# Kernel optimization log

Hardware: AMD Instinct MI355X
Metric: run time of the kernel (lower is better)

## Reference

```python
import jax, jax.numpy as jnp
import numpy as np

C = 128
B = 64
EPS = 1e-6


def _ln2d(x, w, b):
    # LayerNorm over channel dim (NAFNet-style LayerNorm2d), eps=1e-6
    mu = x.mean(axis=1, keepdims=True)
    var = ((x - mu) ** 2).mean(axis=1, keepdims=True)
    return (x - mu) / jnp.sqrt(var + EPS) * w[None, :, None, None] + b[None, :, None, None]


def _conv4(x, w, b):
    # Conv2d kernel 4, stride 4, no padding; NCHW / OIHW
    y = jax.lax.conv_general_dilated(x, w, (4, 4), 'VALID',
                                     dimension_numbers=('NCHW', 'OIHW', 'NCHW'))
    return y + b[None, :, None, None]


def _pixel_shuffle4(x):
    # (B, c*16, H, W) -> (B, c, 4H, 4W), torch PixelShuffle semantics
    b, c16, h, w = x.shape
    c = c16 // 16
    x = x.reshape(b, c, 4, 4, h, w)
    x = x.transpose(0, 1, 4, 2, 5, 3)
    return x.reshape(b, c, h * 4, w * 4)


def setup_inputs() -> dict:
    key = jax.random.key(0)
    ks = jax.random.split(key, 16)
    s = 0.02
    return {
        'x_l': jax.random.normal(ks[0], (B, C, 32, 32), jnp.float32),
        'x_r': jax.random.normal(ks[1], (B, C, 32, 32), jnp.float32),
        'ln_w_l': jnp.ones((C,), jnp.float32), 'ln_b_l': jnp.zeros((C,), jnp.float32),
        'ln_w_r': jnp.ones((C,), jnp.float32), 'ln_b_r': jnp.zeros((C,), jnp.float32),
        'Wl1': jax.random.normal(ks[2], (C, C, 4, 4), jnp.float32) * s,
        'bl1': jnp.zeros((C,), jnp.float32),
        'Wr1': jax.random.normal(ks[3], (C, C, 4, 4), jnp.float32) * s,
        'br1': jnp.zeros((C,), jnp.float32),
        'Wl2': jax.random.normal(ks[4], (C, C, 4, 4), jnp.float32) * s,
        'bl2': jnp.zeros((C,), jnp.float32),
        'Wr2': jax.random.normal(ks[5], (C, C, 4, 4), jnp.float32) * s,
        'br2': jnp.zeros((C,), jnp.float32),
        'pos': jax.random.normal(ks[6], (1, C, 8, 8), jnp.float32),
        'beta': jax.random.normal(ks[7], (1, C, 1, 1), jnp.float32) * s,
        'gamma': jax.random.normal(ks[8], (1, C, 1, 1), jnp.float32) * s,
        'Wl3': jax.random.normal(ks[9], (16 * C, C), jnp.float32) * s,
        'bl3': jnp.zeros((16 * C,), jnp.float32),
        'Wr3': jax.random.normal(ks[10], (16 * C, C), jnp.float32) * s,
        'br3': jnp.zeros((16 * C,), jnp.float32),
    }


def reference(x_l, x_r, ln_w_l, ln_b_l, ln_w_r, ln_b_r, Wl1, bl1, Wr1, br1,
              Wl2, bl2, Wr2, br2, pos, beta, gamma, Wl3, bl3, Wr3, br3):
    c = x_l.shape[1]
    scale = c ** (-0.5)
    B1 = x_l.shape[0]
    B2 = x_r.shape[0]

    Ql = _conv4(_ln2d(x_l, ln_w_l, ln_b_l), Wl1, bl1) + pos  # (B1,c,8,8)
    Qr = _conv4(_ln2d(x_r, ln_w_r, ln_b_r), Wr1, br1) + pos  # (B2,c,8,8)
    h1, w1 = Ql.shape[-2], Ql.shape[-1]
    h2, w2 = Qr.shape[-2], Qr.shape[-1]
    m1, m2 = h1 * w1, h2 * w2

    Qlm = Ql.transpose(0, 2, 3, 1).reshape(B1, m1, c)          # b (h w) c
    Qrm = Qr.transpose(1, 0, 2, 3).reshape(c, B2 * m2)         # c (b h w)
    Vl = (_conv4(x_l, Wl2, bl2) + pos).transpose(0, 2, 3, 1).reshape(B1 * m1, c)
    Vr = (_conv4(x_r, Wr2, br2) + pos).transpose(0, 2, 3, 1).reshape(B2 * m2, c)

    attn = jnp.matmul(Qlm, Qrm) * scale                        # (B1, m1, B2*m2)

    F_r2l = jnp.matmul(jax.nn.softmax(attn * (B2 ** (-0.5)), axis=-1), Vr)
    F_r2l = F_r2l.reshape(B1, h1, w1, c)

    attn2 = attn.reshape(B1, m1, B2, m2).transpose(2, 3, 0, 1).reshape(B2, m2, B1 * m1)
    F_l2r = jnp.matmul(jax.nn.softmax(attn2 * (B1 ** (-0.5)), axis=-1), Vl)
    F_l2r = F_l2r.reshape(B2, h2, w2, c)

    F_r2l = _pixel_shuffle4((jnp.matmul(F_r2l, Wl3.T) + bl3).transpose(0, 3, 1, 2)) * beta
    F_l2r = _pixel_shuffle4((jnp.matmul(F_l2r, Wr3.T) + br3).transpose(0, 3, 1, 2)) * gamma
    return (x_l + F_r2l, x_r + F_l2r)
```

## Files before the change

kernel.cpp:

```cpp
#include <hip/hip_runtime.h>
#include <stdint.h>

using bf16x8 = __attribute__((ext_vector_type(8))) short;
using f32x4  = __attribute__((ext_vector_type(4))) float;

__device__ __forceinline__ unsigned short f2bf(float f) {
  union { float f; uint32_t u; } v; v.f = f;
  uint32_t r = v.u + 0x7FFFu + ((v.u >> 16) & 1u);
  return (unsigned short)(r >> 16);
}
__device__ __forceinline__ uint32_t pk2(float a, float b) {
  return (uint32_t)f2bf(a) | ((uint32_t)f2bf(b) << 16);
}
__device__ __forceinline__ float bf2f(unsigned short s) {
  union { uint32_t u; float f; } v; v.u = ((uint32_t)s) << 16;
  return v.f;
}
__device__ __forceinline__ f32x4 mfma16(bf16x8 a, bf16x8 b, f32x4 c) {
  return __builtin_amdgcn_mfma_f32_16x16x32_bf16(a, b, c, 0, 0, 0);
}

__global__ __launch_bounds__(256) void k_lnstats(
    const float* __restrict__ xl, const float* __restrict__ xr,
    float* __restrict__ muW, float* __restrict__ rsW)
{
  const int bx = blockIdx.x;
  const int side = bx >> 7, rem = bx & 127;
  const int b = rem >> 1, half = rem & 1;
  const float* x = (side ? xr : xl) + (size_t)b * 131072 + half * 512;
  const int t = threadIdx.x;
  const int px = t * 2;
  float s0=0, s1=0, q0=0, q1=0;
#pragma unroll 4
  for (int c = 0; c < 128; ++c) {
    const float2 v = *(const float2*)(x + c*1024 + px);
    s0 += v.x; q0 += v.x*v.x;
    s1 += v.y; q1 += v.y*v.y;
  }
  const int o = (side*64 + b)*1024 + half*512 + px;
  float2 mu, rs;
  mu.x = s0*(1.0f/128.0f); mu.y = s1*(1.0f/128.0f);
  rs.x = rsqrtf(fmaxf(q0*(1.0f/128.0f) - mu.x*mu.x, 0.0f) + 1e-6f);
  rs.y = rsqrtf(fmaxf(q1*(1.0f/128.0f) - mu.y*mu.y, 0.0f) + 1e-6f);
  *(float2*)(muW + o) = mu;
  *(float2*)(rsW + o) = rs;
}

__global__ __launch_bounds__(256) void k_wprep(
    const float* __restrict__ lnwl, const float* __restrict__ lnbl,
    const float* __restrict__ lnwr, const float* __restrict__ lnbr,
    const float* __restrict__ Wl1, const float* __restrict__ bl1,
    const float* __restrict__ Wr1, const float* __restrict__ br1,
    const float* __restrict__ Wl2, const float* __restrict__ Wr2,
    unsigned short* __restrict__ Wq, unsigned short* __restrict__ Wv,
    float* __restrict__ bqW)
{
  const int bx = blockIdx.x;
  const int side = bx >> 7, co = bx & 127;
  const float* W1  = side ? Wr1 : Wl1;
  const float* W2  = side ? Wr2 : Wl2;
  const float* b1  = side ? br1 : bl1;
  const float* lnw = side ? lnwr : lnwl;
  const float* lnb = side ? lnbr : lnbl;
  const int t = threadIdx.x;
  const int ci = t >> 1;
  const float lw = lnw[ci], lb = lnb[ci];

  const size_t dsto = (size_t)(side*32 + (t>>3))*8192 + (size_t)co*64 + (t&7)*8;

  const float* src1 = W1 + (size_t)co*2048 + t*8;
  const float4 a0 = *(const float4*)(src1);
  const float4 a1 = *(const float4*)(src1 + 4);
  float part = (a0.x+a0.y+a0.z+a0.w + a1.x+a1.y+a1.z+a1.w) * lb;
  uint4 pkq;
  pkq.x = pk2(a0.x*lw, a0.y*lw); pkq.y = pk2(a0.z*lw, a0.w*lw);
  pkq.z = pk2(a1.x*lw, a1.y*lw); pkq.w = pk2(a1.z*lw, a1.w*lw);
  *(uint4*)(Wq + dsto) = pkq;

  const float* src2 = W2 + (size_t)co*2048 + t*8;
  const float4 c0 = *(const float4*)(src2);
  const float4 c1 = *(const float4*)(src2 + 4);
  uint4 pkv;
  pkv.x = pk2(c0.x, c0.y); pkv.y = pk2(c0.z, c0.w);
  pkv.z = pk2(c1.x, c1.y); pkv.w = pk2(c1.z, c1.w);
  *(uint4*)(Wv + dsto) = pkv;

  __shared__ float red[4];
  float v = part;
  v += __shfl_down(v, 32, 64); v += __shfl_down(v, 16, 64);
  v += __shfl_down(v, 8, 64);  v += __shfl_down(v, 4, 64);
  v += __shfl_down(v, 2, 64);  v += __shfl_down(v, 1, 64);
  if ((t & 63) == 0) red[t >> 6] = v;
  __syncthreads();
  if (t == 0) bqW[side*128 + co] = b1[co] + red[0] + red[1] + red[2] + red[3];
}

__global__ __launch_bounds__(256) void k_w3prep(
    const float* __restrict__ Wl3, const float* __restrict__ Wr3,
    unsigned short* __restrict__ W3bf)
{
  const int b = blockIdx.x;
  const float* src = (b < 256 ? Wl3 : Wr3) + (size_t)(b & 255) * 1024;
  const int t = threadIdx.x;
  const float4 v = *(const float4*)(src + t*4);
  *(uint2*)(W3bf + (size_t)b*1024 + t*4) = make_uint2(pk2(v.x, v.y), pk2(v.z, v.w));
}

__global__ __launch_bounds__(256) void k_conv(
    const float* __restrict__ xl, const float* __restrict__ xr,
    const unsigned short* __restrict__ Wq, const unsigned short* __restrict__ Wv,
    const float* __restrict__ muW, const float* __restrict__ rsW,
    unsigned short* __restrict__ Cpart)
{
  const int bid = blockIdx.x;
  const int ks = bid & 3;
  const int img = (bid >> 2) & 63;
  const int ctype = bid >> 8;
  const int side = ctype & 1;
  const bool isQ = ctype < 2;
  const float* x = (side ? xr : xl) + (size_t)img * 131072;
  const unsigned short* Bsrc = (isQ ? Wq : Wv) + (size_t)side * 262144;

  const int t = threadIdx.x;
  const int w = t >> 6, l = t & 63, lo = l & 15, g = l >> 4;

  __shared__ __align__(16) unsigned char lds[24576];
  unsigned char* A = lds;
  unsigned char* B = lds + 8192;

  const int cl   = t >> 6;
  const int px0  = (t & 63) * 16;
  const int y    = px0 >> 5;
  const int wr   = y & 3;
  const int pbase = (y >> 2)*8 + ((px0 & 31) >> 2);

  float4 mu4[4], rs4[4];
  if (isQ) {
    const int o = (side*64 + img)*1024 + px0;
#pragma unroll
    for (int i = 0; i < 4; ++i) {
      mu4[i] = *(const float4*)(muW + o + 4*i);
      rs4[i] = *(const float4*)(rsW + o + 4*i);
    }
  }

  const int cout = t >> 1, part = t & 1;
  const int keyB = ((cout ^ (cout >> 3)) & 7) << 4;

  f32x4 acc[4][2];
#pragma unroll
  for (int a = 0; a < 4; ++a) { acc[a][0] = (f32x4)0.0f; acc[a][1] = (f32x4)0.0f; }

  for (int it = 0; it < 8; ++it) {
    const int kb = ks*8 + it;
    __syncthreads();
    {
      const float* xs = x + (size_t)(kb*4 + cl)*1024 + px0;
#pragma unroll
      for (int i = 0; i < 4; ++i) {
        float4 v = *(const float4*)(xs + 4*i);
        if (isQ) {
          v.x = (v.x - mu4[i].x)*rs4[i].x; v.y = (v.y - mu4[i].y)*rs4[i].y;
          v.z = (v.z - mu4[i].z)*rs4[i].z; v.w = (v.w - mu4[i].w)*rs4[i].w;
        }
        const int p = pbase + i;
        int dst = p*128 + cl*32 + wr*8;
        dst ^= ((p ^ (p >> 3)) & 7) << 4;
        *(uint2*)(A + dst) = make_uint2(pk2(v.x, v.y), pk2(v.z, v.w));
      }
    }
    {
      const unsigned short* bs = Bsrc + (size_t)kb*8192 + t*32;
#pragma unroll
      for (int i = 0; i < 4; ++i) {
        const bf16x8 v = *(const bf16x8*)(bs + i*8);
        *(bf16x8*)(B + cout*128 + ((part*64 + i*16) ^ keyB)) = v;
      }
    }
    __syncthreads();
    bf16x8 af[4][2], bfr[2][2];
#pragma unroll
    for (int mf = 0; mf < 4; ++mf) {
      const int row = mf*16 + lo;
      const int key = ((row ^ (row >> 3)) & 7) << 4;
#pragma unroll
      for (int kc = 0; kc < 2; ++kc)
        af[mf][kc] = *(const bf16x8*)(A + row*128 + ((kc*64 + g*16) ^ key));
    }
#pragma unroll
    for (int nf = 0; nf < 2; ++nf) {
      const int row = w*32 + nf*16 + lo;
      const int key = ((row ^ (row >> 3)) & 7) << 4;
#pragma unroll
      for (int kc = 0; kc < 2; ++kc)
        bfr[nf][kc] = *(const bf16x8*)(B + row*128 + ((kc*64 + g*16) ^ key));
    }
    __builtin_amdgcn_s_setprio(1);
#pragma unroll
    for (int kc = 0; kc < 2; ++kc)
#pragma unroll
      for (int nf = 0; nf < 2; ++nf)
#pragma unroll
        for (int mf = 0; mf < 4; ++mf)
          acc[mf][nf] = mfma16(af[mf][kc], bfr[nf][kc], acc[mf][nf]);
    __builtin_amdgcn_s_setprio(0);
  }

  unsigned short* Cp = Cpart + (size_t)bid * 8192;
#pragma unroll
  for (int mf = 0; mf < 4; ++mf)
#pragma unroll
    for (int nf = 0; nf < 2; ++nf) {
      const int c = w*32 + nf*16 + lo;
      const int p0 = mf*16 + g*4;
      *(uint2*)(Cp + c*64 + p0) =
          make_uint2(pk2(acc[mf][nf][0], acc[mf][nf][1]),
                     pk2(acc[mf][nf][2], acc[mf][nf][3]));
    }
}

__global__ __launch_bounds__(256) void k_convred(
    const unsigned short* __restrict__ Cpart,
    const float* __restrict__ bqW,
    const float* __restrict__ bl2, const float* __restrict__ br2,
    const float* __restrict__ pos,
    unsigned short* __restrict__ Qbf, unsigned short* __restrict__ Vtbf)
{
  const int bid2 = blockIdx.x;
  const int ctype = bid2 >> 6, img = bid2 & 63;
  const int side = ctype & 1;
  const bool isQ = ctype < 2;
  const int t = threadIdx.x;

  __shared__ float S[64][130];

  const int c = t >> 1, p0 = (t & 1) * 32;
  {
    float acc[32];
#pragma unroll
    for (int j = 0; j < 32; ++j) acc[j] = 0.f;
#pragma unroll
    for (int s = 0; s < 4; ++s) {
      const unsigned short* Cp = Cpart + ((size_t)(bid2*4 + s))*8192 + c*64 + p0;
#pragma unroll
      for (int j8 = 0; j8 < 4; ++j8) {
        const bf16x8 v = *(const bf16x8*)(Cp + j8*8);
#pragma unroll
        for (int e = 0; e < 8; ++e)
          acc[j8*8 + e] += bf2f((unsigned short)v[e]);
      }
    }
#pragma unroll
    for (int j = 0; j < 32; ++j) S[p0 + j][c] = acc[j];
  }
  __syncthreads();

  if (isQ) {
    const float* bq = bqW + side*128;
    const int p = t >> 2, c0 = (t & 3) * 32;
    const int rot = (t & 3) * 4;
    uint32_t pk[16];
#pragma unroll
    for (int j2 = 0; j2 < 16; ++j2) {
      const int jj = (j2 + rot) & 15;
      const int ca = c0 + jj*2;
      const float2 sv = *(const float2*)(&S[p][ca]);
      const float va = (sv.x + bq[ca]     + pos[ca*64 + p])     * 0.105112052f;
      const float vb = (sv.y + bq[ca + 1] + pos[(ca+1)*64 + p]) * 0.105112052f;
      pk[jj] = pk2(va, vb);
    }
    unsigned short* Qo = Qbf + (size_t)side*524288 + ((size_t)(img*64 + p))*128 + c0;
    *(uint4*)(Qo)      = make_uint4(pk[0],  pk[1],  pk[2],  pk[3]);
    *(uint4*)(Qo + 8)  = make_uint4(pk[4],  pk[5],  pk[6],  pk[7]);
    *(uint4*)(Qo + 16) = make_uint4(pk[8],  pk[9],  pk[10], pk[11]);
    *(uint4*)(Qo + 24) = make_uint4(pk[12], pk[13], pk[14], pk[15]);
  } else {
    const float* b2 = side ? br2 : bl2;
    const float bb = b2[c];
    uint32_t pk[16];
#pragma unroll
    for (int j2 = 0; j2 < 16; ++j2) {
      const int pa = p0 + j2*2;
      const float va = S[pa][c]     + bb + pos[c*64 + pa];
      const float vb = S[pa + 1][c] + bb + pos[c*64 + pa + 1];
      pk[j2] = pk2(va, vb);
    }
    unsigned short* Vo = Vtbf + (size_t)side*524288 + (size_t)c*4096 + img*64 + p0;
    *(uint4*)(Vo)      = make_uint4(pk[0],  pk[1],  pk[2],  pk[3]);
    *(uint4*)(Vo + 8)  = make_uint4(pk[4],  pk[5],  pk[6],  pk[7]);
    *(uint4*)(Vo + 16) = make_uint4(pk[8],  pk[9],  pk[10], pk[11]);
    *(uint4*)(Vo + 24) = make_uint4(pk[12], pk[13], pk[14], pk[15]);
  }
}

__global__ __launch_bounds__(256, 2) void k_attn(
    const unsigned short* __restrict__ Qbf,
    const unsigned short* __restrict__ Vtbf,
    float* __restrict__ Opart,
    float* __restrict__ Lpart)
{
  const int bid = blockIdx.x;
  const int xcd = bid & 7;
  const int dir = xcd >> 2;
  const int ks  = xcd & 3;
  const int qb  = bid >> 3;
  const unsigned short* Qp = Qbf  + (size_t)dir*524288;
  const unsigned short* Kp = Qbf  + (size_t)(1-dir)*524288;
  const unsigned short* Vp = Vtbf + (size_t)(1-dir)*524288;

  const int t = threadIdx.x;
  const int w = t >> 6, l = t & 63, lo = l & 15, g = l >> 4;

  __shared__ __align__(16) unsigned char lds[73728];
  unsigned char* ldsP = lds + 65536;
  __shared__ float lred[4][64];

  bf16x8 aq[4][4];
#pragma unroll
  for (int mf = 0; mf < 4; ++mf)
#pragma unroll
    for (int kc = 0; kc < 4; ++kc)
      aq[mf][kc] = *(const bf16x8*)(Qp + (size_t)(qb*64 + mf*16 + lo)*128 + kc*32 + g*8);

  f32x4 o[4][2];
#pragma unroll
  for (int a = 0; a < 4; ++a) { o[a][0] = (f32x4)0.0f; o[a][1] = (f32x4)0.0f; }
  float ls[4][4] = {{0,0,0,0},{0,0,0,0},{0,0,0,0},{0,0,0,0}};

  const int kt0 = ks * 16;

  const int ksrcBase = t ^ ((t >> 4) & 7);
  const int vc    = t >> 3;
  const int vi16  = (t & 7) * 16;
  const int vsoff = (vi16 ^ (((t >> 3) & 7) << 4)) >> 1;

  {
    const uint4* src = (const uint4*)(Kp + (size_t)kt0*8192);
#pragma unroll
    for (int j = 0; j < 4; ++j)
      *(uint4*)(lds + (t + 256*j)*16) = src[ksrcBase + 256*j];
#pragma unroll
    for (int j = 0; j < 4; ++j) {
      const int c = vc + 32*j;
      *(uint4*)(lds + 32768 + c*128 + vi16) =
          *(const uint4*)(Vp + (size_t)c*4096 + kt0*64 + vsoff);
    }
  }
  __syncthreads();

  for (int it = 0; it < 16; ++it) {
    const int cur = it & 1;
    unsigned char* curK = lds + cur*16384;
    unsigned char* curV = lds + 32768 + cur*16384;

    uint4 kr0, kr1, kr2, kr3, vr0, vr1, vr2, vr3;
    if (it < 15) {
      const int kt = kt0 + it + 1;
      const uint4* src = (const uint4*)(Kp + (size_t)kt*8192);
      kr0 = src[ksrcBase];
      kr1 = src[ksrcBase + 256];
      kr2 = src[ksrcBase + 512];
      kr3 = src[ksrcBase + 768];
      const unsigned short* vsrc = Vp + (size_t)kt*64 + vsoff;
      vr0 = *(const uint4*)(vsrc + (size_t)(vc     )*4096);
      vr1 = *(const uint4*)(vsrc + (size_t)(vc + 32)*4096);
      vr2 = *(const uint4*)(vsrc + (size_t)(vc + 64)*4096);
      vr3 = *(const uint4*)(vsrc + (size_t)(vc + 96)*4096);
    }

    f32x4 s[4];
    s[0] = (f32x4)0.0f; s[1] = (f32x4)0.0f; s[2] = (f32x4)0.0f; s[3] = (f32x4)0.0f;
    const int krow = w*16 + lo;
    const int keyk = (krow & 7) << 4;
    __builtin_amdgcn_s_setprio(1);
#pragma unroll
    for (int kc = 0; kc < 4; ++kc) {
      const bf16x8 bk = *(const bf16x8*)(curK + krow*256 + ((kc*64 + g*16) ^ keyk));
#pragma unroll
      for (int mf = 0; mf < 4; ++mf)
        s[mf] = mfma16(aq[mf][kc], bk, s[mf]);
    }
    __builtin_amdgcn_s_setprio(0);

#pragma unroll
    for (int mf = 0; mf < 4; ++mf)
#pragma unroll
      for (int rr = 0; rr < 4; ++rr) {
        const float e = __expf(s[mf][rr]);
        ls[mf][rr] += e;
        const int q = mf*16 + g*4 + rr;
        const int inrow = (w*32 + lo*2) ^ ((q & 7) << 4);
        *(unsigned short*)(ldsP + q*128 + inrow) = f2bf(e);
      }
    __syncthreads();

    __builtin_amdgcn_s_setprio(1);
#pragma unroll
    for (int kd = 0; kd < 2; ++kd) {
      bf16x8 pa[4];
#pragma unroll
      for (int mf = 0; mf < 4; ++mf) {
        const int q = mf*16 + lo;
        pa[mf] = *(const bf16x8*)(ldsP + q*128 + ((kd*64 + g*16) ^ ((q & 7) << 4)));
      }
#pragma unroll
      for (int nf = 0; nf < 2; ++nf) {
        const int c = w*32 + nf*16 + lo;
        const bf16x8 bv = *(const bf16x8*)(curV + c*128 + ((kd*64 + g*16) ^ ((c & 7) << 4)));
#pragma unroll
        for (int mf = 0; mf < 4; ++mf)
          o[mf][nf] = mfma16(pa[mf], bv, o[mf][nf]);
      }
    }
    __builtin_amdgcn_s_setprio(0);

    if (it < 15) {
      unsigned char* nK = lds + (cur ^ 1)*16384;
      unsigned char* nV = lds + 32768 + (cur ^ 1)*16384;
      *(uint4*)(nK + (t      )*16) = kr0;
      *(uint4*)(nK + (t + 256)*16) = kr1;
      *(uint4*)(nK + (t + 512)*16) = kr2;
      *(uint4*)(nK + (t + 768)*16) = kr3;
      *(uint4*)(nV + (vc     )*128 + vi16) = vr0;
      *(uint4*)(nV + (vc + 32)*128 + vi16) = vr1;
      *(uint4*)(nV + (vc + 64)*128 + vi16) = vr2;
      *(uint4*)(nV + (vc + 96)*128 + vi16) = vr3;
    }
    __syncthreads();
  }

#pragma unroll
  for (int mf = 0; mf < 4; ++mf)
#pragma unroll
    for (int rr = 0; rr < 4; ++rr) {
      float v = ls[mf][rr];
      v += __shfl_xor(v, 1, 64);
      v += __shfl_xor(v, 2, 64);
      v += __shfl_xor(v, 4, 64);
      v += __shfl_xor(v, 8, 64);
      ls[mf][rr] = v;
    }
  if (lo == 0) {
#pragma unroll
    for (int mf = 0; mf < 4; ++mf)
#pragma unroll
      for (int rr = 0; rr < 4; ++rr)
        lred[w][mf*16 + g*4 + rr] = ls[mf][rr];
  }
  __syncthreads();

  float* Ob = Opart + (((size_t)dir*64 + qb)*4 + ks)*64*128;
#pragma unroll
  for (int mf = 0; mf < 4; ++mf)
#pragma unroll
    for (int nf = 0; nf < 2; ++nf) {
      const int c = w*32 + nf*16 + lo;
#pragma unroll
      for (int rr = 0; rr < 4; ++rr) {
        const int q = mf*16 + g*4 + rr;
        Ob[q*128 + c] = o[mf][nf][rr];
      }
    }
  if (t < 64)
    Lpart[(((size_t)dir*64 + qb)*4 + ks)*64 + t] =
        lred[0][t] + lred[1][t] + lred[2][t] + lred[3][t];
}

__global__ __launch_bounds__(256) void k_reduce(
    const float* __restrict__ Opart, const float* __restrict__ Lpart,
    unsigned short* __restrict__ Fbf)
{
  const int bid = blockIdx.x;
  const int dir = bid >> 7, rb = bid & 127;
  const int t = threadIdx.x;
  const int qr = t >> 3;
  const int cs = (t & 7) * 16;
  const int r  = rb*32 + qr;
  const int qb = r >> 6, q = r & 63;
  const size_t pb = ((size_t)dir*64 + qb)*4;
  float acc[16];
#pragma unroll
  for (int i = 0; i < 16; ++i) acc[i] = 0.f;
  float lsum = 0.f;
#pragma unroll
  for (int s = 0; s < 4; ++s) {
    const float* Ob = Opart + ((pb + s)*64 + q)*128 + cs;
#pragma unroll
    for (int i = 0; i < 16; i += 4) {
      const float4 v = *(const float4*)(Ob + i);
      acc[i] += v.x; acc[i+1] += v.y; acc[i+2] += v.z; acc[i+3] += v.w;
    }
    lsum += Lpart[(pb + s)*64 + q];
  }
  const float inv = 1.0f / lsum;
  uint32_t pkw[8];
#pragma unroll
  for (int i = 0; i < 8; ++i) pkw[i] = pk2(acc[2*i]*inv, acc[2*i+1]*inv);
  unsigned short* Fo = Fbf + (size_t)dir*524288 + (size_t)r*128 + cs;
  *(uint4*)(Fo)     = make_uint4(pkw[0], pkw[1], pkw[2], pkw[3]);
  *(uint4*)(Fo + 8) = make_uint4(pkw[4], pkw[5], pkw[6], pkw[7]);
}

__global__ __launch_bounds__(256) void k_proj(
    const unsigned short* __restrict__ Fbf,
    const unsigned short* __restrict__ W3bf,
    const float* __restrict__ bl3, const float* __restrict__ br3,
    const float* __restrict__ beta, const float* __restrict__ gamma,
    const float* __restrict__ xl, const float* __restrict__ xr,
    float* __restrict__ out)
{
  const int nb = blockIdx.x, mb = blockIdx.y, side = blockIdx.z;
  const unsigned short* F  = Fbf + (size_t)side*524288 + (size_t)mb*8192;
  const unsigned short* W3 = W3bf + (size_t)side*262144 + (size_t)nb*16384;
  const float* b3  = (side ? br3 : bl3) + nb*128;
  const float* scl = side ? gamma : beta;
  const float* xin = (side ? xr : xl) + (size_t)mb*131072;
  float* op = out + (size_t)side*8388608 + (size_t)mb*131072;

  const int t = threadIdx.x;
  const int w = t >> 6, l = t & 63, lo = l & 15, g = l >> 4;

  __shared__ __align__(16) unsigned char lds[49152];
  unsigned char* Ft = lds;
  unsigned char* B3 = lds + 16384;
  float* Sf = (float*)lds;

  {
    const uint4* src = (const uint4*)F;
#pragma unroll
    for (int j = 0; j < 4; ++j) {
      const int idx = t + 256*j;
      const int dst = idx*16;
      const int row = dst >> 8;
      *(uint4*)(Ft + dst) = src[(dst ^ ((row & 7) << 4)) >> 4];
    }
  }
  {
    const int nl = t >> 1, half = t & 1;
    const unsigned short* wsrc = W3 + (size_t)nl*128 + half*64;
#pragma unroll
    for (int ch = 0; ch < 8; ++ch) {
      const uint4 v = *(const uint4*)(wsrc + ch*8);
      const int inrow = (half*128 + ch*16) ^ ((nl & 7) << 4);
      *(uint4*)(B3 + nl*256 + inrow) = v;
    }
  }
  __syncthreads();

  f32x4 acc[4][2];
#pragma unroll
  for (int a=0;a<4;a++) { acc[a][0] = (f32x4)0.0f; acc[a][1] = (f32x4)0.0f; }

  bf16x8 af[4][4];
#pragma unroll
  for (int mf = 0; mf < 4; ++mf) {
    const int row = mf*16 + lo;
#pragma unroll
    for (int kc = 0; kc < 4; ++kc)
      af[mf][kc] = *(const bf16x8*)(Ft + row*256 + ((kc*64 + g*16) ^ ((row & 7) << 4)));
  }
#pragma unroll
  for (int kc = 0; kc < 4; ++kc)
#pragma unroll
    for (int nf = 0; nf < 2; ++nf) {
      const int n = w*32 + nf*16 + lo;
      const bf16x8 bb = *(const bf16x8*)(B3 + n*256 + ((kc*64 + g*16) ^ ((n & 7) << 4)));
#pragma unroll
      for (int mf = 0; mf < 4; ++mf)
        acc[mf][nf] = mfma16(af[mf][kc], bb, acc[mf][nf]);
    }

  __syncthreads();

  {
    const int r4 = (lo >> 2) & 3, sc = lo & 3;
#pragma unroll
    for (int nf = 0; nf < 2; ++nf) {
      const int cl = w*2 + nf;
      const int n16 = w*32 + nf*16 + lo;
      const float scc = scl[nb*8 + cl];
      const float bb3 = b3[n16];
#pragma unroll
      for (int mf = 0; mf < 4; ++mf)
#pragma unroll
        for (int rr = 0; rr < 4; ++rr) {
          const int pi = mf*16 + g*4 + rr;
          const int h = pi >> 3, wc = pi & 7;
          Sf[cl*1032 + h*128 + r4*32 + wc*4 + sc] = scc*(acc[mf][nf][rr] + bb3);
        }
    }
  }
  __syncthreads();

#pragma unroll
  for (int j = 0; j < 8; ++j) {
    const int pix = t*4;
    const float4 s = *(const float4*)(Sf + j*1032 + pix);
    const size_t gaddr = (size_t)(nb*8 + j)*1024 + pix;
    const float4 xv = *(const float4*)(xin + gaddr);
    float4 r;
    r.x = xv.x + s.x; r.y = xv.y + s.y; r.z = xv.z + s.z; r.w = xv.w + s.w;
    *(float4*)(op + gaddr) = r;
  }
}

extern "C" void kernel_launch(void* const* d_in, const int* in_sizes, int n_in,
                              void* d_out, int out_size, void* d_ws, size_t ws_size,
                              hipStream_t stream) {
  (void)in_sizes; (void)n_in; (void)out_size; (void)ws_size;
  const float* xl   = (const float*)d_in[0];
  const float* xr   = (const float*)d_in[1];
  const float* lnwl = (const float*)d_in[2];
  const float* lnbl = (const float*)d_in[3];
  const float* lnwr = (const float*)d_in[4];
  const float* lnbr = (const float*)d_in[5];
  const float* Wl1  = (const float*)d_in[6];
  const float* bl1  = (const float*)d_in[7];
  const float* Wr1  = (const float*)d_in[8];
  const float* br1  = (const float*)d_in[9];
  const float* Wl2  = (const float*)d_in[10];
  const float* bl2  = (const float*)d_in[11];
  const float* Wr2  = (const float*)d_in[12];
  const float* br2  = (const float*)d_in[13];
  const float* pos  = (const float*)d_in[14];
  const float* beta = (const float*)d_in[15];
  const float* gamma= (const float*)d_in[16];
  const float* Wl3  = (const float*)d_in[17];
  const float* bl3  = (const float*)d_in[18];
  const float* Wr3  = (const float*)d_in[19];
  const float* br3  = (const float*)d_in[20];

  float* muW = (float*)d_ws;
  float* rsW = muW + 131072;
  float* bqW = rsW + 131072;
  unsigned short* Wq   = (unsigned short*)(bqW + 256);
  unsigned short* Wv   = Wq + 524288;
  unsigned short* Qbf  = Wv + 524288;
  unsigned short* Vtbf = Qbf + 1048576;
  unsigned short* Fbf  = Vtbf + 1048576;
  unsigned short* W3bf = Fbf + 1048576;
  unsigned short* Cpart = W3bf + 524288;
  float* Opart = (float*)Cpart;
  float* Lpart = (float*)(Cpart + 8388608);

  k_lnstats<<<256, 256, 0, stream>>>(xl, xr, muW, rsW);
  k_wprep<<<256, 256, 0, stream>>>(lnwl, lnbl, lnwr, lnbr,
      Wl1, bl1, Wr1, br1, Wl2, Wr2, Wq, Wv, bqW);
  k_w3prep<<<512, 256, 0, stream>>>(Wl3, Wr3, W3bf);
  k_conv<<<1024, 256, 0, stream>>>(xl, xr, Wq, Wv, muW, rsW, Cpart);
  k_convred<<<256, 256, 0, stream>>>(Cpart, bqW, bl2, br2, pos, Qbf, Vtbf);
  k_attn<<<512, 256, 0, stream>>>(Qbf, Vtbf, Opart, Lpart);
  k_reduce<<<256, 256, 0, stream>>>(Opart, Lpart, Fbf);
  k_proj<<<dim3(16, 64, 2), 256, 0, stream>>>(Fbf, W3bf, bl3, br3,
      beta, gamma, xl, xr, (float*)d_out);
}
```

Before: 124.9 us.

## Merge prep kernels into one launch and transpose score MFMA for packed P stores

Folds the LN-stats, conv-weight prep and projection-weight prep kernels into a single launch, removing two launch gaps. In attention the QK^T MFMA operands are swapped so each lane holds four consecutive keys of one query. The exp values can then be stored to LDS as one packed 8-byte write instead of four scalar 2-byte writes, and the row-sum reduction needs fewer shuffles. The Q scale gains a log2(e) factor so exp2f replaces __expf; this relies on matching swizzle and layout, and the merged kernel keeps a __syncthreads inside only one branch.

```diff
diff --git a/kernel.cpp b/kernel.cpp
--- a/kernel.cpp
+++ b/kernel.cpp
@@ -20,90 +20,85 @@
   return __builtin_amdgcn_mfma_f32_16x16x32_bf16(a, b, c, 0, 0, 0);
 }
 
-__global__ __launch_bounds__(256) void k_lnstats(
+__global__ __launch_bounds__(256) void k_prep(
     const float* __restrict__ xl, const float* __restrict__ xr,
-    float* __restrict__ muW, float* __restrict__ rsW)
-{
-  const int bx = blockIdx.x;
-  const int side = bx >> 7, rem = bx & 127;
-  const int b = rem >> 1, half = rem & 1;
-  const float* x = (side ? xr : xl) + (size_t)b * 131072 + half * 512;
-  const int t = threadIdx.x;
-  const int px = t * 2;
-  float s0=0, s1=0, q0=0, q1=0;
-#pragma unroll 4
-  for (int c = 0; c < 128; ++c) {
-    const float2 v = *(const float2*)(x + c*1024 + px);
-    s0 += v.x; q0 += v.x*v.x;
-    s1 += v.y; q1 += v.y*v.y;
-  }
-  const int o = (side*64 + b)*1024 + half*512 + px;
-  float2 mu, rs;
-  mu.x = s0*(1.0f/128.0f); mu.y = s1*(1.0f/128.0f);
-  rs.x = rsqrtf(fmaxf(q0*(1.0f/128.0f) - mu.x*mu.x, 0.0f) + 1e-6f);
-  rs.y = rsqrtf(fmaxf(q1*(1.0f/128.0f) - mu.y*mu.y, 0.0f) + 1e-6f);
-  *(float2*)(muW + o) = mu;
-  *(float2*)(rsW + o) = rs;
-}
-
-__global__ __launch_bounds__(256) void k_wprep(
     const float* __restrict__ lnwl, const float* __restrict__ lnbl,
     const float* __restrict__ lnwr, const float* __restrict__ lnbr,
     const float* __restrict__ Wl1, const float* __restrict__ bl1,
     const float* __restrict__ Wr1, const float* __restrict__ br1,
     const float* __restrict__ Wl2, const float* __restrict__ Wr2,
+    const float* __restrict__ Wl3, const float* __restrict__ Wr3,
+    float* __restrict__ muW, float* __restrict__ rsW,
     unsigned short* __restrict__ Wq, unsigned short* __restrict__ Wv,
-    float* __restrict__ bqW)
+    float* __restrict__ bqW, unsigned short* __restrict__ W3bf)
 {
-  const int bx = blockIdx.x;
-  const int side = bx >> 7, co = bx & 127;
-  const float* W1  = side ? Wr1 : Wl1;
-  const float* W2  = side ? Wr2 : Wl2;
-  const float* b1  = side ? br1 : bl1;
-  const float* lnw = side ? lnwr : lnwl;
-  const float* lnb = side ? lnbr : lnbl;
+  const int gbid = blockIdx.x;
   const int t = threadIdx.x;
-  const int ci = t >> 1;
-  const float lw = lnw[ci], lb = lnb[ci];
-
-  const size_t dsto = (size_t)(side*32 + (t>>3))*8192 + (size_t)co*64 + (t&7)*8;
-
-  const float* src1 = W1 + (size_t)co*2048 + t*8;
-  const float4 a0 = *(const float4*)(src1);
-  const float4 a1 = *(const float4*)(src1 + 4);
-  float part = (a0.x+a0.y+a0.z+a0.w + a1.x+a1.y+a1.z+a1.w) * lb;
-  uint4 pkq;
-  pkq.x = pk2(a0.x*lw, a0.y*lw); pkq.y = pk2(a0.z*lw, a0.w*lw);
-  pkq.z = pk2(a1.x*lw, a1.y*lw); pkq.w = pk2(a1.z*lw, a1.w*lw);
-  *(uint4*)(Wq + dsto) = pkq;
-
-  const float* src2 = W2 + (size_t)co*2048 + t*8;
-  const float4 c0 = *(const float4*)(src2);
-  const float4 c1 = *(const float4*)(src2 + 4);
-  uint4 pkv;
-  pkv.x = pk2(c0.x, c0.y); pkv.y = pk2(c0.z, c0.w);
-  pkv.z = pk2(c1.x, c1.y); pkv.w = pk2(c1.z, c1.w);
-  *(uint4*)(Wv + dsto) = pkv;
-
   __shared__ float red[4];
-  float v = part;
-  v += __shfl_down(v, 32, 64); v += __shfl_down(v, 16, 64);
-  v += __shfl_down(v, 8, 64);  v += __shfl_down(v, 4, 64);
-  v += __shfl_down(v, 2, 64);  v += __shfl_down(v, 1, 64);
-  if ((t & 63) == 0) red[t >> 6] = v;
-  __syncthreads();
-  if (t == 0) bqW[side*128 + co] = b1[co] + red[0] + red[1] + red[2] + red[3];
-}
-
-__global__ __launch_bounds__(256) void k_w3prep(
-    const float* __restrict__ Wl3, const float* __restrict__ Wr3,
-    unsigned short* __restrict__ W3bf)
-{
-  const int b = blockIdx.x;
-  const float* src = (b < 256 ? Wl3 : Wr3) + (size_t)(b & 255) * 1024;
-  const int t = threadIdx.x;
-  const float4 v = *(const float4*)(src + t*4);
-  *(uint2*)(W3bf + (size_t)b*1024 + t*4) = make_uint2(pk2(v.x, v.y), pk2(v.z, v.w));
+
+  if (gbid < 256) {
+    const int bx = gbid;
+    const int side = bx >> 7, rem = bx & 127;
+    const int b = rem >> 1, half = rem & 1;
+    const float* x = (side ? xr : xl) + (size_t)b * 131072 + half * 512;
+    const int px = t * 2;
+    float s0=0, s1=0, q0=0, q1=0;
+#pragma unroll 4
+    for (int c = 0; c < 128; ++c) {
+      const float2 v = *(const float2*)(x + c*1024 + px);
+      s0 += v.x; q0 += v.x*v.x;
+      s1 += v.y; q1 += v.y*v.y;
+    }
+    const int o = (side*64 + b)*1024 + half*512 + px;
+    float2 mu, rs;
+    mu.x = s0*(1.0f/128.0f); mu.y = s1*(1.0f/128.0f);
+    rs.x = rsqrtf(fmaxf(q0*(1.0f/128.0f) - mu.x*mu.x, 0.0f) + 1e-6f);
+    rs.y = rsqrtf(fmaxf(q1*(1.0f/128.0f) - mu.y*mu.y, 0.0f) + 1e-6f);
+    *(float2*)(muW + o) = mu;
+    *(float2*)(rsW + o) = rs;
+  } else if (gbid < 512) {
+    const int bx = gbid - 256;
+    const int side = bx >> 7, co = bx & 127;
+    const float* W1  = side ? Wr1 : Wl1;
+    const float* W2  = side ? Wr2 : Wl2;
+    const float* b1  = side ? br1 : bl1;
+    const float* lnw = side ? lnwr : lnwl;
+    const float* lnb = side ? lnbr : lnbl;
+    const int ci = t >> 1;
+    const float lw = lnw[ci], lb = lnb[ci];
+
+    const size_t dsto = (size_t)(side*32 + (t>>3))*8192 + (size_t)co*64 + (t&7)*8;
+
+    const float* src1 = W1 + (size_t)co*2048 + t*8;
+    const float4 a0 = *(const float4*)(src1);
+    const float4 a1 = *(const float4*)(src1 + 4);
+    float part = (a0.x+a0.y+a0.z+a0.w + a1.x+a1.y+a1.z+a1.w) * lb;
+    uint4 pkq;
+    pkq.x = pk2(a0.x*lw, a0.y*lw); pkq.y = pk2(a0.z*lw, a0.w*lw);
+    pkq.z = pk2(a1.x*lw, a1.y*lw); pkq.w = pk2(a1.z*lw, a1.w*lw);
+    *(uint4*)(Wq + dsto) = pkq;
+
+    const float* src2 = W2 + (size_t)co*2048 + t*8;
+    const float4 c0 = *(const float4*)(src2);
+    const float4 c1 = *(const float4*)(src2 + 4);
+    uint4 pkv;
+    pkv.x = pk2(c0.x, c0.y); pkv.y = pk2(c0.z, c0.w);
+    pkv.z = pk2(c1.x, c1.y); pkv.w = pk2(c1.z, c1.w);
+    *(uint4*)(Wv + dsto) = pkv;
+
+    float v = part;
+    v += __shfl_down(v, 32, 64); v += __shfl_down(v, 16, 64);
+    v += __shfl_down(v, 8, 64);  v += __shfl_down(v, 4, 64);
+    v += __shfl_down(v, 2, 64);  v += __shfl_down(v, 1, 64);
+    if ((t & 63) == 0) red[t >> 6] = v;
+    __syncthreads();
+    if (t == 0) bqW[side*128 + co] = b1[co] + red[0] + red[1] + red[2] + red[3];
+  } else {
+    const int b = gbid - 512;
+    const float* src = (b < 256 ? Wl3 : Wr3) + (size_t)(b & 255) * 1024;
+    const float4 v = *(const float4*)(src + t*4);
+    *(uint2*)(W3bf + (size_t)b*1024 + t*4) = make_uint2(pk2(v.x, v.y), pk2(v.z, v.w));
+  }
 }
 
 __global__ __launch_bounds__(256) void k_conv(
@@ -265,8 +260,8 @@
       const int jj = (j2 + rot) & 15;
       const int ca = c0 + jj*2;
       const float2 sv = *(const float2*)(&S[p][ca]);
-      const float va = (sv.x + bq[ca]     + pos[ca*64 + p])     * 0.105112052f;
-      const float vb = (sv.y + bq[ca + 1] + pos[(ca+1)*64 + p]) * 0.105112052f;
+      const float va = (sv.x + bq[ca]     + pos[ca*64 + p])     * 0.12625283f;
+      const float vb = (sv.y + bq[ca + 1] + pos[(ca+1)*64 + p]) * 0.12625283f;
       pk[jj] = pk2(va, vb);
     }
     unsigned short* Qo = Qbf + (size_t)side*524288 + ((size_t)(img*64 + p))*128 + c0;
@@ -325,7 +320,7 @@
   f32x4 o[4][2];
 #pragma unroll
   for (int a = 0; a < 4; ++a) { o[a][0] = (f32x4)0.0f; o[a][1] = (f32x4)0.0f; }
-  float ls[4][4] = {{0,0,0,0},{0,0,0,0},{0,0,0,0},{0,0,0,0}};
+  float ls[4] = {0.f, 0.f, 0.f, 0.f};
 
   const int kt0 = ks * 16;
 
@@ -378,20 +373,21 @@
       const bf16x8 bk = *(const bf16x8*)(curK + krow*256 + ((kc*64 + g*16) ^ keyk));
 #pragma unroll
       for (int mf = 0; mf < 4; ++mf)
-        s[mf] = mfma16(aq[mf][kc], bk, s[mf]);
+        s[mf] = mfma16(bk, aq[mf][kc], s[mf]);
     }
     __builtin_amdgcn_s_setprio(0);
 
 #pragma unroll
-    for (int mf = 0; mf < 4; ++mf)
-#pragma unroll
-      for (int rr = 0; rr < 4; ++rr) {
-        const float e = __expf(s[mf][rr]);
-        ls[mf][rr] += e;
-        const int q = mf*16 + g*4 + rr;
-        const int inrow = (w*32 + lo*2) ^ ((q & 7) << 4);
-        *(unsigned short*)(ldsP + q*128 + inrow) = f2bf(e);
-      }
+    for (int mf = 0; mf < 4; ++mf) {
+      const float e0 = exp2f(s[mf][0]);
+      const float e1 = exp2f(s[mf][1]);
+      const float e2 = exp2f(s[mf][2]);
+      const float e3 = exp2f(s[mf][3]);
+      ls[mf] += (e0 + e1) + (e2 + e3);
+      const int q = mf*16 + lo;
+      const int koff = (w*32 + g*8) ^ ((q & 7) << 4);
+      *(uint2*)(ldsP + q*128 + koff) = make_uint2(pk2(e0, e1), pk2(e2, e3));
+    }
     __syncthreads();
 
     __builtin_amdgcn_s_setprio(1);
@@ -430,22 +426,11 @@
   }
 
 #pragma unroll
-  for (int mf = 0; mf < 4; ++mf)
-#pragma unroll
-    for (int rr = 0; rr < 4; ++rr) {
-      float v = ls[mf][rr];
-      v += __shfl_xor(v, 1, 64);
-      v += __shfl_xor(v, 2, 64);
-      v += __shfl_xor(v, 4, 64);
-      v += __shfl_xor(v, 8, 64);
-      ls[mf][rr] = v;
-    }
-  if (lo == 0) {
-#pragma unroll
-    for (int mf = 0; mf < 4; ++mf)
-#pragma unroll
-      for (int rr = 0; rr < 4; ++rr)
-        lred[w][mf*16 + g*4 + rr] = ls[mf][rr];
+  for (int mf = 0; mf < 4; ++mf) {
+    float v = ls[mf];
+    v += __shfl_xor(v, 16, 64);
+    v += __shfl_xor(v, 32, 64);
+    if (l < 16) lred[w][mf*16 + lo] = v;
   }
   __syncthreads();
 
@@ -643,10 +628,8 @@
   float* Opart = (float*)Cpart;
   float* Lpart = (float*)(Cpart + 8388608);
 
-  k_lnstats<<<256, 256, 0, stream>>>(xl, xr, muW, rsW);
-  k_wprep<<<256, 256, 0, stream>>>(lnwl, lnbl, lnwr, lnbr,
-      Wl1, bl1, Wr1, br1, Wl2, Wr2, Wq, Wv, bqW);
-  k_w3prep<<<512, 256, 0, stream>>>(Wl3, Wr3, W3bf);
+  k_prep<<<1024, 256, 0, stream>>>(xl, xr, lnwl, lnbl, lnwr, lnbr,
+      Wl1, bl1, Wr1, br1, Wl2, Wr2, Wl3, Wr3, muW, rsW, Wq, Wv, bqW, W3bf);
   k_conv<<<1024, 256, 0, stream>>>(xl, xr, Wq, Wv, muW, rsW, Cpart);
   k_convred<<<256, 256, 0, stream>>>(Cpart, bqW, bl2, br2, pos, Qbf, Vtbf);
   k_attn<<<512, 256, 0, stream>>>(Qbf, Vtbf, Opart, Lpart);
```

Measured after the change: 123.1 us (median of 2 runs). No clear change (-1.5%).
